# Kernel optimization log

Measured on AMD Instinct MI355X. Metric: run time of the kernel, lower is better.

Reference implementation:

```python
import jax, jax.numpy as jnp
import numpy as np

NX = 41                      # cube side: 2*r_max/voxel + 1 with r_max=6.0, voxel=0.3
VOXEL = 0.3
R_MAX = 6.0
MIN_DIST = 0.8
MIN_SEP = max(1, int(round(MIN_DIST / VOXEL)))   # 3 voxels
K = 4                        # topk_per_channel
NEG = -1.0e9                 # fp32 sentinel used by the torch module
VALID_THRESH = -1.0e8


def setup_inputs() -> dict:
    key = jax.random.key(0)
    B, N, C = 1, 128, 4
    G = NX ** 3
    ax = np.arange(NX)
    ii, jj, kk = np.meshgrid(ax, ax, ax, indexing='ij')
    coords = np.stack([ii, jj, kk], axis=-1).reshape(-1, 3)          # [G,3] integer voxel coords
    center = (NX - 1) / 2.0
    grid_xyz = ((coords - center) * VOXEL).astype(np.float32)        # [G,3] local Angstrom coords
    sphere_mask = np.linalg.norm(grid_xyz, axis=-1) <= R_MAX         # [G] bool
    k1, k2, k3 = jax.random.split(key, 3)
    density = jax.random.normal(k1, (B, N, C, G), jnp.float32)
    A = jax.random.normal(k2, (B, N, 3, 3), jnp.float32)
    Rmats, _ = jnp.linalg.qr(A)                                      # proper-ish rotation matrices
    tpos = jax.random.normal(k3, (B, N, 3), jnp.float32)
    node_mask = jnp.ones((B, N), jnp.float32)
    return dict(density=density,
                grid_xyz=jnp.asarray(grid_xyz),
                sphere_mask=jnp.asarray(sphere_mask),
                coords_int=jnp.asarray(coords, jnp.int32),
                Rmats=Rmats, tpos=tpos, node_mask=node_mask)


def extract_peaks(density, grid_xyz, sphere_mask, coords_int):
    # density: [B,N,C,G]; iterative argmax peak-picking with Chebyshev NMS suppression.
    v0 = jnp.where(sphere_mask[None, None, None, :], density, NEG)
    cx = coords_int[:, 0][None, None, None, :]   # [1,1,1,G]
    cy = coords_int[:, 1][None, None, None, :]
    cz = coords_int[:, 2][None, None, None, :]

    def step(v, _):
        idx = jnp.argmax(v, axis=-1)                                   # [B,N,C]
        score = jnp.take_along_axis(v, idx[..., None], axis=-1)[..., 0]
        valid = score > VALID_THRESH
        xyz = grid_xyz[idx]                                            # [B,N,C,3]
        ijk = coords_int[idx]                                          # [B,N,C,3]
        # Chebyshev (max-abs) voxel distance to the picked peak, per axis to avoid a [.,G,3] temp
        d = jnp.maximum(jnp.maximum(jnp.abs(cx - ijk[..., 0:1]),
                                    jnp.abs(cy - ijk[..., 1:2])),
                        jnp.abs(cz - ijk[..., 2:3]))                    # [B,N,C,G]
        suppress = (d <= MIN_SEP) & valid[..., None]
        v = jnp.where(suppress, NEG, v)
        out = (jnp.where(valid, score, NEG),
               jnp.where(valid[..., None], xyz, 0.0),
               valid)
        return v, out

    _, (scores, xyz, mask) = jax.lax.scan(step, v0, None, length=K)
    # K is leading scan axis -> move to axis 3 giving [B,N,C,K,...]
    return (jnp.moveaxis(xyz, 0, 3), jnp.moveaxis(scores, 0, 3), jnp.moveaxis(mask, 0, 3))


def reference(density, grid_xyz, sphere_mask, coords_int, Rmats, tpos, node_mask):
    peaks_xyz, peaks_score, peaks_mask = extract_peaks(density, grid_xyz, sphere_mask, coords_int)
    # local -> global frame: R @ x + t
    coords_global = jnp.einsum('bnij,bnckj->bncki', Rmats, peaks_xyz) + tpos[:, :, None, None, :]
    m = node_mask[..., None, None, None]                                # [B,N,1,1,1]
    coords_local = peaks_xyz * m
    coords_global = coords_global * m
    scores = peaks_score * node_mask[..., None, None]
    mask = peaks_mask & node_mask.astype(bool)[..., None, None]
    return coords_local, coords_global, scores, mask
```

## Files before the change

### kernel.cpp

```cpp
#include <hip/hip_runtime.h>

#define G_VOX  68921
#define GMAX   68920
#define NSEG   272
#define MWORDS 2176
#define NEGV (-1.0e9f)
#define VTH  (-1.0e8f)

__device__ __forceinline__ bool sphere_bit(const float* __restrict__ gxyz, int e) {
    if (e >= G_VOX) return false;
    float gx = gxyz[e * 3 + 0];
    float gy = gxyz[e * 3 + 1];
    float gz = gxyz[e * 3 + 2];
    float s  = __fadd_rn(__fadd_rn(__fmul_rn(gx, gx), __fmul_rn(gy, gy)),
                         __fmul_rn(gz, gz));
    return (__fsqrt_rn(s) <= 6.0f);
}

__global__ __launch_bounds__(256) void build_mask(
    const float* __restrict__ gxyz, unsigned int* __restrict__ mask)
{
    int idx = blockIdx.x * 256 + threadIdx.x;
    unsigned long long bal = __ballot(sphere_bit(gxyz, idx));
    int lane = threadIdx.x & 63;
    if (lane == 0)       mask[idx >> 5] = (unsigned int)bal;
    else if (lane == 32) mask[idx >> 5] = (unsigned int)(bal >> 32);
}

__global__ __launch_bounds__(512) void fused_peaks(
    const float* __restrict__ density,
    const float* __restrict__ gxyz,
    const unsigned int* __restrict__ maskg,
    const float* __restrict__ Rm, const float* __restrict__ tp,
    const float* __restrict__ nmask,
    float* __restrict__ out)
{
    __shared__ unsigned int smask[MWORDS + 2];
    __shared__ float sval[NSEG];
    __shared__ int   sidx[NSEG];
    __shared__ int   flag[NSEG];
    __shared__ int   list[104];
    __shared__ int   nlist;
    __shared__ float rv[8];
    __shared__ int   ri[8];
    __shared__ float pval[4];
    __shared__ int   pidx[4];
    __shared__ int   pki[4], pkj[4], pkk[4];

    const int tid  = threadIdx.x;
    const int nc   = blockIdx.x;
    const int n    = nc >> 2;
    const int h    = (-nc) & 3;
    const int lane = tid & 63;
    const int w    = tid >> 6;
    const float* dens = density + (size_t)nc * G_VOX;

    for (int i = tid; i < MWORDS + 2; i += 512) smask[i] = (i < MWORDS) ? maskg[i] : 0u;
    for (int i = tid; i < NSEG; i += 512) flag[i] = 0;
    __syncthreads();

    for (int j = 0; j < 34; ++j) {
        const int s = w + 8 * j;
        const int e = h + 4 * tid + 2048 * j;
        const int wd = e >> 5, sh = e & 31;
        unsigned long long mw = ((unsigned long long)smask[wd + 1] << 32) | smask[wd];
        const unsigned int bits = (unsigned int)(mw >> sh) & 0xFu;

        float bv = NEGV;
        int   bi = e;
        if (bits) {
            if (e + 3 <= GMAX) {
                float4 d = *reinterpret_cast<const float4*>(dens + e);
                float v0 = (bits & 1u) ? d.x : NEGV;
                float v1 = (bits & 2u) ? d.y : NEGV;
                float v2 = (bits & 4u) ? d.z : NEGV;
                float v3 = (bits & 8u) ? d.w : NEGV;
                if (v0 > bv) { bv = v0; bi = e;     }
                if (v1 > bv) { bv = v1; bi = e + 1; }
                if (v2 > bv) { bv = v2; bi = e + 2; }
                if (v3 > bv) { bv = v3; bi = e + 3; }
            } else {
                #pragma unroll
                for (int u = 0; u < 4; ++u) {
                    if (((bits >> u) & 1u) && e + u <= GMAX) {
                        float v = dens[e + u];
                        if (v > bv) { bv = v; bi = e + u; }
                    }
                }
            }
        }
        #pragma unroll
        for (int off = 32; off > 0; off >>= 1) {
            float ov = __shfl_down(bv, off);
            int   oi = __shfl_down(bi, off);
            if (ov > bv || (ov == bv && oi < bi)) { bv = ov; bi = oi; }
        }
        if (lane == 0) { sval[s] = bv; sidx[s] = bi; }
    }
    __syncthreads();

    for (int p = 0; p < 4; ++p) {
        float bv = -INFINITY;
        int   bi = 0x7FFFFFFF;
        if (tid < NSEG) { bv = sval[tid]; bi = sidx[tid]; }
        #pragma unroll
        for (int off = 32; off > 0; off >>= 1) {
            float ov = __shfl_down(bv, off);
            int   oi = __shfl_down(bi, off);
            if (ov > bv || (ov == bv && oi < bi)) { bv = ov; bi = oi; }
        }
        if (lane == 0) { rv[w] = bv; ri[w] = bi; }
        __syncthreads();
        if (w == 0) {
            bv = (lane < 8) ? rv[lane] : -INFINITY;
            bi = (lane < 8) ? ri[lane] : 0x7FFFFFFF;
            #pragma unroll
            for (int off = 4; off > 0; off >>= 1) {
                float ov = __shfl_down(bv, off);
                int   oi = __shfl_down(bi, off);
                if (ov > bv || (ov == bv && oi < bi)) { bv = ov; bi = oi; }
            }
            if (lane == 0) {
                pval[p] = bv;
                pidx[p] = bi;
                int pi = bi / 1681;
                int rr = bi - pi * 1681;
                int pj = rr / 41;
                pki[p] = pi; pkj[p] = pj; pkk[p] = rr - pj * 41;
                nlist = 0;
            }
        }
        __syncthreads();

        if (p < 3 && pval[p] > VTH) {
            if (tid < 49) {
                int di = tid / 7 - 3, dj = tid % 7 - 3;
                int ii = pki[p] + di, jj = pkj[p] + dj;
                if (ii >= 0 && ii <= 40 && jj >= 0 && jj <= 40) {
                    int k0 = pkk[p] - 3; if (k0 < 0)  k0 = 0;
                    int k1 = pkk[p] + 3; if (k1 > 40) k1 = 40;
                    int b0  = ii * 1681 + jj * 41 + k0;
                    int cnt = k1 - k0 + 1;
                    unsigned long long m = ((1ull << cnt) - 1ull) << (b0 & 31);
                    int w0 = b0 >> 5;
                    atomicAnd(&smask[w0], ~(unsigned int)m);
                    unsigned int hi = (unsigned int)(m >> 32);
                    if (hi) atomicAnd(&smask[w0 + 1], ~hi);
                    int s0 = (b0 > h) ? (b0 - h) >> 8 : 0;
                    int s1 = (b0 + cnt - 1 > h) ? (b0 + cnt - 1 - h) >> 8 : 0;
                    if (atomicMax(&flag[s0], p + 1) < p + 1) {
                        int q = atomicAdd(&nlist, 1); list[q] = s0;
                    }
                    if (s1 != s0 && atomicMax(&flag[s1], p + 1) < p + 1) {
                        int q = atomicAdd(&nlist, 1); list[q] = s1;
                    }
                }
            }
            __syncthreads();
            const int cnt = nlist;
            for (int q = w; q < cnt; q += 8) {
                const int s = list[q];
                const int e = h + 256 * s + 4 * lane;
                const int wd = e >> 5, sh = e & 31;
                unsigned long long mw = ((unsigned long long)smask[wd + 1] << 32) | smask[wd];
                const unsigned int bits = (unsigned int)(mw >> sh) & 0xFu;
                float bv2 = NEGV;
                int   bi2 = e;
                if (bits) {
                    if (e + 3 <= GMAX) {
                        float4 d = *reinterpret_cast<const float4*>(dens + e);
                        float v0 = (bits & 1u) ? d.x : NEGV;
                        float v1 = (bits & 2u) ? d.y : NEGV;
                        float v2 = (bits & 4u) ? d.z : NEGV;
                        float v3 = (bits & 8u) ? d.w : NEGV;
                        if (v0 > bv2) { bv2 = v0; bi2 = e;     }
                        if (v1 > bv2) { bv2 = v1; bi2 = e + 1; }
                        if (v2 > bv2) { bv2 = v2; bi2 = e + 2; }
                        if (v3 > bv2) { bv2 = v3; bi2 = e + 3; }
                    } else {
                        #pragma unroll
                        for (int u = 0; u < 4; ++u) {
                            if (((bits >> u) & 1u) && e + u <= GMAX) {
                                float v = dens[e + u];
                                if (v > bv2) { bv2 = v; bi2 = e + u; }
                            }
                        }
                    }
                }
                #pragma unroll
                for (int off = 32; off > 0; off >>= 1) {
                    float ov = __shfl_down(bv2, off);
                    int   oi = __shfl_down(bi2, off);
                    if (ov > bv2 || (ov == bv2 && oi < bi2)) { bv2 = ov; bi2 = oi; }
                }
                if (lane == 0) { sval[s] = bv2; sidx[s] = bi2; }
            }
        }
        __syncthreads();
    }

    if (tid < 4) {
        const int k   = tid;
        const float val = pval[k];
        const int   idx = pidx[k];
        const bool valid = val > VTH;
        float gx = 0.0f, gy = 0.0f, gz = 0.0f;
        if (valid) {
            gx = gxyz[idx * 3 + 0];
            gy = gxyz[idx * 3 + 1];
            gz = gxyz[idx * 3 + 2];
        }
        const float nm = nmask[n];
        const float* R = Rm + n * 9;
        const float* t = tp + n * 3;
        float wx = R[0] * gx + R[1] * gy + R[2] * gz + t[0];
        float wy = R[3] * gx + R[4] * gy + R[5] * gz + t[1];
        float wz = R[6] * gx + R[7] * gy + R[8] * gz + t[2];

        const size_t o3 = ((size_t)nc * 4 + k) * 3;
        out[o3 + 0] = gx * nm;
        out[o3 + 1] = gy * nm;
        out[o3 + 2] = gz * nm;
        out[6144 + o3 + 0] = wx * nm;
        out[6144 + o3 + 1] = wy * nm;
        out[6144 + o3 + 2] = wz * nm;
        const size_t o1 = (size_t)nc * 4 + k;
        out[12288 + o1] = (valid ? val : NEGV) * nm;
        out[14336 + o1] = (valid && nm != 0.0f) ? 1.0f : 0.0f;
    }
}

extern "C" void kernel_launch(void* const* d_in, const int* in_sizes, int n_in,
                              void* d_out, int out_size, void* d_ws, size_t ws_size,
                              hipStream_t stream) {
    const float* density  = (const float*)d_in[0];
    const float* grid_xyz = (const float*)d_in[1];
    const float* Rm    = (const float*)d_in[4];
    const float* tpos  = (const float*)d_in[5];
    const float* nmask = (const float*)d_in[6];
    float* out = (float*)d_out;

    unsigned int* mask = (unsigned int*)d_ws;

    build_mask<<<dim3(272), dim3(256), 0, stream>>>(grid_xyz, mask);
    fused_peaks<<<dim3(512), dim3(512), 0, stream>>>(density, grid_xyz, mask,
                                                     Rm, tpos, nmask, out);
}
```

Baseline: 229.6 us.

## Widen segments to 1024 voxels with precomputed 16-bit per-lane sphere masks

Each wave segment now covers 1024 voxels (four float4 loads per lane) instead of 256, so there are 68 segments instead of 272. This shrinks the cross-wave reduction: the final stage now combines 2 partials instead of 8. The mask-building kernel also precomputes a per-lane 16-bit sphere mask for every phase offset, so the initial scan reads one ushort instead of doing shared-memory bit extraction. Rescans after suppression still read the shared mask, but each dirty segment now costs four times as many loads. The larger segments also leave waves with uneven work.

```diff
diff --git a/kernel.cpp b/kernel.cpp
--- a/kernel.cpp
+++ b/kernel.cpp
@@ -2,8 +2,9 @@
 
 #define G_VOX  68921
 #define GMAX   68920
-#define NSEG   272
+#define NSEG   68
 #define MWORDS 2176
+#define RMQ_P  4352
 #define NEGV (-1.0e9f)
 #define VTH  (-1.0e8f)
 
@@ -18,19 +19,40 @@
 }
 
 __global__ __launch_bounds__(256) void build_mask(
-    const float* __restrict__ gxyz, unsigned int* __restrict__ mask)
+    const float* __restrict__ gxyz,
+    unsigned int* __restrict__ mask,
+    unsigned short* __restrict__ rmq)
 {
-    int idx = blockIdx.x * 256 + threadIdx.x;
-    unsigned long long bal = __ballot(sphere_bit(gxyz, idx));
-    int lane = threadIdx.x & 63;
-    if (lane == 0)       mask[idx >> 5] = (unsigned int)bal;
-    else if (lane == 32) mask[idx >> 5] = (unsigned int)(bal >> 32);
+    const int tid  = threadIdx.x;
+    const int lane = tid & 63;
+    {
+        int idx = blockIdx.x * 256 + tid;
+        unsigned long long bal = __ballot(sphere_bit(gxyz, idx));
+        if (lane == 0)       mask[idx >> 5] = (unsigned int)bal;
+        else if (lane == 32) mask[idx >> 5] = (unsigned int)(bal >> 32);
+    }
+    int gid = blockIdx.x * 256 + tid;
+    if (gid < 4 * RMQ_P) {
+        int h    = gid / RMQ_P;
+        int rem  = gid - h * RMQ_P;
+        int s    = rem >> 6;
+        int p    = rem & 63;
+        int base = h + 1024 * s + 4 * p;
+        unsigned int bits = 0;
+        #pragma unroll
+        for (int j = 0; j < 4; ++j)
+            #pragma unroll
+            for (int u = 0; u < 4; ++u)
+                if (sphere_bit(gxyz, base + 256 * j + u)) bits |= 1u << (j * 4 + u);
+        rmq[gid] = (unsigned short)bits;
+    }
 }
 
 __global__ __launch_bounds__(512) void fused_peaks(
     const float* __restrict__ density,
     const float* __restrict__ gxyz,
     const unsigned int* __restrict__ maskg,
+    const unsigned short* __restrict__ rmq,
     const float* __restrict__ Rm, const float* __restrict__ tp,
     const float* __restrict__ nmask,
     float* __restrict__ out)
@@ -56,35 +78,35 @@
     const float* dens = density + (size_t)nc * G_VOX;
 
     for (int i = tid; i < MWORDS + 2; i += 512) smask[i] = (i < MWORDS) ? maskg[i] : 0u;
-    for (int i = tid; i < NSEG; i += 512) flag[i] = 0;
-    __syncthreads();
-
-    for (int j = 0; j < 34; ++j) {
-        const int s = w + 8 * j;
-        const int e = h + 4 * tid + 2048 * j;
-        const int wd = e >> 5, sh = e & 31;
-        unsigned long long mw = ((unsigned long long)smask[wd + 1] << 32) | smask[wd];
-        const unsigned int bits = (unsigned int)(mw >> sh) & 0xFu;
-
+    if (tid < NSEG) flag[tid] = 0;
+
+    for (int s = w; s < NSEG; s += 8) {
+        const unsigned int bits16 = rmq[h * RMQ_P + s * 64 + lane];
+        const int eb = h + 1024 * s + 4 * lane;
         float bv = NEGV;
-        int   bi = e;
-        if (bits) {
-            if (e + 3 <= GMAX) {
-                float4 d = *reinterpret_cast<const float4*>(dens + e);
-                float v0 = (bits & 1u) ? d.x : NEGV;
-                float v1 = (bits & 2u) ? d.y : NEGV;
-                float v2 = (bits & 4u) ? d.z : NEGV;
-                float v3 = (bits & 8u) ? d.w : NEGV;
-                if (v0 > bv) { bv = v0; bi = e;     }
-                if (v1 > bv) { bv = v1; bi = e + 1; }
-                if (v2 > bv) { bv = v2; bi = e + 2; }
-                if (v3 > bv) { bv = v3; bi = e + 3; }
-            } else {
-                #pragma unroll
-                for (int u = 0; u < 4; ++u) {
-                    if (((bits >> u) & 1u) && e + u <= GMAX) {
-                        float v = dens[e + u];
-                        if (v > bv) { bv = v; bi = e + u; }
+        int   bi = eb;
+        #pragma unroll
+        for (int j = 0; j < 4; ++j) {
+            const unsigned int b4 = (bits16 >> (4 * j)) & 0xFu;
+            const int e = eb + 256 * j;
+            if (b4) {
+                if (e + 3 <= GMAX) {
+                    float4 d = *reinterpret_cast<const float4*>(dens + e);
+                    float v0 = (b4 & 1u) ? d.x : NEGV;
+                    float v1 = (b4 & 2u) ? d.y : NEGV;
+                    float v2 = (b4 & 4u) ? d.z : NEGV;
+                    float v3 = (b4 & 8u) ? d.w : NEGV;
+                    if (v0 > bv) { bv = v0; bi = e;     }
+                    if (v1 > bv) { bv = v1; bi = e + 1; }
+                    if (v2 > bv) { bv = v2; bi = e + 2; }
+                    if (v3 > bv) { bv = v3; bi = e + 3; }
+                } else {
+                    #pragma unroll
+                    for (int u = 0; u < 4; ++u) {
+                        if (((b4 >> u) & 1u) && e + u <= GMAX) {
+                            float v = dens[e + u];
+                            if (v > bv) { bv = v; bi = e + u; }
+                        }
                     }
                 }
             }
@@ -112,14 +134,11 @@
         if (lane == 0) { rv[w] = bv; ri[w] = bi; }
         __syncthreads();
         if (w == 0) {
-            bv = (lane < 8) ? rv[lane] : -INFINITY;
-            bi = (lane < 8) ? ri[lane] : 0x7FFFFFFF;
-            #pragma unroll
-            for (int off = 4; off > 0; off >>= 1) {
-                float ov = __shfl_down(bv, off);
-                int   oi = __shfl_down(bi, off);
-                if (ov > bv || (ov == bv && oi < bi)) { bv = ov; bi = oi; }
-            }
+            bv = (lane < 2) ? rv[lane] : -INFINITY;
+            bi = (lane < 2) ? ri[lane] : 0x7FFFFFFF;
+            float ov = __shfl_down(bv, 1);
+            int   oi = __shfl_down(bi, 1);
+            if (ov > bv || (ov == bv && oi < bi)) { bv = ov; bi = oi; }
             if (lane == 0) {
                 pval[p] = bv;
                 pidx[p] = bi;
@@ -146,8 +165,8 @@
                     atomicAnd(&smask[w0], ~(unsigned int)m);
                     unsigned int hi = (unsigned int)(m >> 32);
                     if (hi) atomicAnd(&smask[w0 + 1], ~hi);
-                    int s0 = (b0 > h) ? (b0 - h) >> 8 : 0;
-                    int s1 = (b0 + cnt - 1 > h) ? (b0 + cnt - 1 - h) >> 8 : 0;
+                    int s0 = (b0 > h) ? (b0 - h) >> 10 : 0;
+                    int s1 = (b0 + cnt - 1 > h) ? (b0 + cnt - 1 - h) >> 10 : 0;
                     if (atomicMax(&flag[s0], p + 1) < p + 1) {
                         int q = atomicAdd(&nlist, 1); list[q] = s0;
                     }
@@ -159,30 +178,34 @@
             __syncthreads();
             const int cnt = nlist;
             for (int q = w; q < cnt; q += 8) {
-                const int s = list[q];
-                const int e = h + 256 * s + 4 * lane;
-                const int wd = e >> 5, sh = e & 31;
-                unsigned long long mw = ((unsigned long long)smask[wd + 1] << 32) | smask[wd];
-                const unsigned int bits = (unsigned int)(mw >> sh) & 0xFu;
+                const int s  = list[q];
+                const int eb = h + 1024 * s + 4 * lane;
                 float bv2 = NEGV;
-                int   bi2 = e;
-                if (bits) {
-                    if (e + 3 <= GMAX) {
-                        float4 d = *reinterpret_cast<const float4*>(dens + e);
-                        float v0 = (bits & 1u) ? d.x : NEGV;
-                        float v1 = (bits & 2u) ? d.y : NEGV;
-                        float v2 = (bits & 4u) ? d.z : NEGV;
-                        float v3 = (bits & 8u) ? d.w : NEGV;
-                        if (v0 > bv2) { bv2 = v0; bi2 = e;     }
-                        if (v1 > bv2) { bv2 = v1; bi2 = e + 1; }
-                        if (v2 > bv2) { bv2 = v2; bi2 = e + 2; }
-                        if (v3 > bv2) { bv2 = v3; bi2 = e + 3; }
-                    } else {
-                        #pragma unroll
-                        for (int u = 0; u < 4; ++u) {
-                            if (((bits >> u) & 1u) && e + u <= GMAX) {
-                                float v = dens[e + u];
-                                if (v > bv2) { bv2 = v; bi2 = e + u; }
+                int   bi2 = eb;
+                #pragma unroll
+                for (int j = 0; j < 4; ++j) {
+                    const int e = eb + 256 * j;
+                    const int wd = e >> 5, sh = e & 31;
+                    unsigned long long mw = ((unsigned long long)smask[wd + 1] << 32) | smask[wd];
+                    const unsigned int b4 = (unsigned int)(mw >> sh) & 0xFu;
+                    if (b4) {
+                        if (e + 3 <= GMAX) {
+                            float4 d = *reinterpret_cast<const float4*>(dens + e);
+                            float v0 = (b4 & 1u) ? d.x : NEGV;
+                            float v1 = (b4 & 2u) ? d.y : NEGV;
+                            float v2 = (b4 & 4u) ? d.z : NEGV;
+                            float v3 = (b4 & 8u) ? d.w : NEGV;
+                            if (v0 > bv2) { bv2 = v0; bi2 = e;     }
+                            if (v1 > bv2) { bv2 = v1; bi2 = e + 1; }
+                            if (v2 > bv2) { bv2 = v2; bi2 = e + 2; }
+                            if (v3 > bv2) { bv2 = v3; bi2 = e + 3; }
+                        } else {
+                            #pragma unroll
+                            for (int u = 0; u < 4; ++u) {
+                                if (((b4 >> u) & 1u) && e + u <= GMAX) {
+                                    float v = dens[e + u];
+                                    if (v > bv2) { bv2 = v; bi2 = e + u; }
+                                }
                             }
                         }
                     }
@@ -240,9 +263,10 @@
     const float* nmask = (const float*)d_in[6];
     float* out = (float*)d_out;
 
-    unsigned int* mask = (unsigned int*)d_ws;
-
-    build_mask<<<dim3(272), dim3(256), 0, stream>>>(grid_xyz, mask);
-    fused_peaks<<<dim3(512), dim3(512), 0, stream>>>(density, grid_xyz, mask,
+    unsigned int*   mask = (unsigned int*)d_ws;
+    unsigned short* rmq  = (unsigned short*)((char*)d_ws + 8704);
+
+    build_mask<<<dim3(272), dim3(256), 0, stream>>>(grid_xyz, mask, rmq);
+    fused_peaks<<<dim3(512), dim3(512), 0, stream>>>(density, grid_xyz, mask, rmq,
                                                      Rm, tpos, nmask, out);
 }
```

Result: slower. 237.2 us (+3.3%).
